# Optimization experiments

Hardware: AMD Instinct MI355X
Metric: run time of the kernel (lower is better)

The kernel has to match this reference:

```python
import jax, jax.numpy as jnp
import numpy as np

B, H, S, D = 2, 16, 2048, 64
DILATION_RATE = 2

def dilated_global_mask(seq_len: int, dilation_rate: int) -> jnp.ndarray:
    # mask[i, j] = 1 if |i - j| % dilation_rate == 0 else 0  -> [S, S] float32
    i = jnp.arange(seq_len)[:, None]
    j = jnp.arange(seq_len)[None, :]
    return ((jnp.abs(i - j) % dilation_rate) == 0).astype(jnp.float32)

def setup_inputs() -> dict:
    key = jax.random.key(0)
    kq, kk, kv = jax.random.split(key, 3)
    queries = jax.random.normal(kq, (B, H, S, D), dtype=jnp.float32)
    keys = jax.random.normal(kk, (B, H, S, D), dtype=jnp.float32)
    values = jax.random.normal(kv, (B, H, S, D), dtype=jnp.float32)
    return {"queries": queries, "keys": keys, "values": values}

def reference(queries, keys, values):
    depth = queries.shape[-1]
    # scores: [B, H, S, S]
    scores = jnp.einsum("bhqd,bhkd->bhqk", queries, keys)
    scores = scores / jnp.sqrt(jnp.asarray(depth, dtype=jnp.float32))
    gmask = dilated_global_mask(keys.shape[-2], DILATION_RATE)  # [S, S]
    # NOTE: multiplicative masking (masked scores become 0, not -inf), as in source
    masked_scores = scores * gmask
    attention_probs = jax.nn.softmax(masked_scores, axis=-1)
    # dropout is identity at inference (training=None)
    out = jnp.einsum("bhqk,bhkd->bhqd", attention_probs, values)
    return out
```

## Files before the change

### kernel.cpp

```cpp
#include <hip/hip_runtime.h>
#include <hip/hip_bf16.h>


#define B_   2
#define H_   16
#define S_   2048
#define D_   64
#define SP_  1024
#define BQ   128
#define BK   64
#define NKT  (SP_ / BK)
#define NW   4

#define QSCALE 0.180336884f

#if __has_builtin(__builtin_amdgcn_exp2f)
#define EXP2(x) __builtin_amdgcn_exp2f(x)
#else
#define EXP2(x) exp2f(x)
#endif

typedef __bf16 bf16x8 __attribute__((ext_vector_type(8)));
typedef __bf16 bf16x4 __attribute__((ext_vector_type(4)));
typedef float  f32x4  __attribute__((ext_vector_type(4)));
typedef short  s16x4  __attribute__((ext_vector_type(4)));

static __device__ __forceinline__ f32x4 mfma16(bf16x4 a, bf16x4 b, f32x4 c) {
    return __builtin_amdgcn_mfma_f32_16x16x16bf16_1k(
        __builtin_bit_cast(s16x4, a), __builtin_bit_cast(s16x4, b), c, 0, 0, 0);
}

#define KSW(r, c8) ((((c8) ^ ((r) & 7)) << 3))

__global__ __launch_bounds__(256, 2) void attn_kernel(const float* __restrict__ Q,
                                                      const float* __restrict__ K,
                                                      const float* __restrict__ V,
                                                      float* __restrict__ out) {
    const int bh  = blockIdx.x;
    const int par = blockIdx.y;
    const int qt  = blockIdx.z;
    const int tid  = threadIdx.x;
    const int lane = tid & 63;
    const int wave = tid >> 6;
    const int l15  = lane & 15;
    const int quad = lane >> 4;

    __shared__ __align__(16) char arena[33792];
    __bf16 (*kbuf)[BK][64] = (__bf16 (*)[BK][64])arena;
    __bf16 (*vbuf)[D_][64] = (__bf16 (*)[D_][64])(arena + 16384);
    float  (*vred)[64]     = (float  (*)[64])(arena + 32768);

    const size_t base = (size_t)bh * S_ * D_;
    const float* Qb = Q + base;
    const float* Kb = K + base;
    const float* Vb = V + base;
    const int vofs = (par == 0) ? D_ : -D_;

    bf16x8 qf[2][2];
    #pragma unroll
    for (int qt2 = 0; qt2 < 2; ++qt2) {
        const int qrow = qt * BQ + wave * 32 + qt2 * 16 + l15;
        const float* qsrc = Qb + (size_t)(par + 2 * qrow) * D_ + quad * 8;
        #pragma unroll
        for (int ks = 0; ks < 2; ++ks) {
            const float4 a = *(const float4*)(qsrc + ks * 32);
            const float4 b = *(const float4*)(qsrc + ks * 32 + 4);
            bf16x8 w;
            w[0] = (__bf16)(a.x * QSCALE); w[1] = (__bf16)(a.y * QSCALE);
            w[2] = (__bf16)(a.z * QSCALE); w[3] = (__bf16)(a.w * QSCALE);
            w[4] = (__bf16)(b.x * QSCALE); w[5] = (__bf16)(b.y * QSCALE);
            w[6] = (__bf16)(b.z * QSCALE); w[7] = (__bf16)(b.w * QSCALE);
            qf[qt2][ks] = w;
        }
    }

    const int kr0 = tid >> 3;
    const int kc8 = tid & 7;

    float4 pka[2], pkb[2];
    float  pv[16], pvo[16];

    auto issue_loads = [&](int kt) {
        #pragma unroll
        for (int i = 0; i < 2; ++i) {
            const int r = i * 32 + kr0;
            const float* ksrc = Kb + (size_t)(par + 2 * (kt * BK + r)) * D_ + kc8 * 8;
            pka[i] = *(const float4*)ksrc;
            pkb[i] = *(const float4*)(ksrc + 4);
        }
        #pragma unroll
        for (int i = 0; i < 2; ++i) {
            const int c = wave + 4 * i;
            const float* vsrc = Vb + (size_t)(par + 2 * (kt * BK + c * 8)) * D_ + lane;
            #pragma unroll
            for (int j = 0; j < 8; ++j) {
                pv [i * 8 + j] = vsrc[(size_t)(2 * j) * D_];
                pvo[i * 8 + j] = vsrc[(size_t)(2 * j) * D_ + vofs];
            }
        }
    };

    float vo = 0.f;
    auto stage = [&](int buf) {
        #pragma unroll
        for (int i = 0; i < 2; ++i) {
            const int r = i * 32 + kr0;
            bf16x8 w;
            w[0] = (__bf16)pka[i].x; w[1] = (__bf16)pka[i].y;
            w[2] = (__bf16)pka[i].z; w[3] = (__bf16)pka[i].w;
            w[4] = (__bf16)pkb[i].x; w[5] = (__bf16)pkb[i].y;
            w[6] = (__bf16)pkb[i].z; w[7] = (__bf16)pkb[i].w;
            *(bf16x8*)&kbuf[buf][r][KSW(r, kc8)] = w;
        }
        #pragma unroll
        for (int i = 0; i < 2; ++i) {
            const int c = wave + 4 * i;
            bf16x8 w;
            #pragma unroll
            for (int j = 0; j < 8; ++j) w[j] = (__bf16)pv[i * 8 + j];
            *(bf16x8*)&vbuf[buf][lane][KSW(lane, c)] = w;
            vo += ((pvo[i*8+0] + pvo[i*8+1]) + (pvo[i*8+2] + pvo[i*8+3]))
                + ((pvo[i*8+4] + pvo[i*8+5]) + (pvo[i*8+6] + pvo[i*8+7]));
        }
    };

    issue_loads(0);
    stage(0);
    __syncthreads();

    f32x4 acc[2][4];
    #pragma unroll
    for (int q2 = 0; q2 < 2; ++q2)
        #pragma unroll
        for (int dt = 0; dt < 4; ++dt) acc[q2][dt] = (f32x4){0.f, 0.f, 0.f, 0.f};
    float l_acc[2] = {0.f, 0.f};

    for (int kt = 0; kt < NKT; ++kt) {
        const int cur = kt & 1;
        const bool pf = (kt + 1 < NKT);

        if (pf) issue_loads(kt + 1);

        const __bf16 (*kb)[64] = kbuf[cur];
        const __bf16 (*vb)[64] = vbuf[cur];

        bf16x8 ka[2][4];
        #pragma unroll
        for (int ks = 0; ks < 2; ++ks)
            #pragma unroll
            for (int kt4 = 0; kt4 < 4; ++kt4) {
                const int R = kt4 * 16 + l15;
                ka[ks][kt4] = *(const bf16x8*)&kb[R][KSW(R, ks * 4 + quad)];
            }
        bf16x4 va[4][4];
        #pragma unroll
        for (int dt = 0; dt < 4; ++dt) {
            const int R = dt * 16 + l15;
            const int ro = R & 7;
            #pragma unroll
            for (int kt4 = 0; kt4 < 4; ++kt4) {
                const int ch = (kt4 * 2 + (quad >> 1)) ^ ro;
                va[kt4][dt] = *(const bf16x4*)&vb[R][ch * 8 + (quad & 1) * 4];
            }
        }

        #pragma unroll
        for (int qt2 = 0; qt2 < 2; ++qt2) {
            f32x4 st[4];
            #pragma unroll
            for (int kt4 = 0; kt4 < 4; ++kt4) st[kt4] = (f32x4){0.f, 0.f, 0.f, 0.f};
            #pragma unroll
            for (int ks = 0; ks < 2; ++ks)
                #pragma unroll
                for (int kt4 = 0; kt4 < 4; ++kt4)
                    st[kt4] = __builtin_amdgcn_mfma_f32_16x16x32_bf16(
                        ka[ks][kt4], qf[qt2][ks], st[kt4], 0, 0, 0);
            #pragma unroll
            for (int kt4 = 0; kt4 < 4; ++kt4) {
                const float p0 = EXP2(st[kt4][0]);
                const float p1 = EXP2(st[kt4][1]);
                const float p2 = EXP2(st[kt4][2]);
                const float p3 = EXP2(st[kt4][3]);
                l_acc[qt2] += (p0 + p1) + (p2 + p3);
                bf16x4 pb;
                pb[0] = (__bf16)p0; pb[1] = (__bf16)p1;
                pb[2] = (__bf16)p2; pb[3] = (__bf16)p3;
                #pragma unroll
                for (int dt = 0; dt < 4; ++dt)
                    acc[qt2][dt] = mfma16(va[kt4][dt], pb, acc[qt2][dt]);
            }
        }

        if (pf) stage(1 - cur);
        __syncthreads();
    }

    vred[wave][lane] = vo;
    __syncthreads();

    f32x4 vs4[4];
    #pragma unroll
    for (int dt = 0; dt < 4; ++dt) {
        f32x4 s = (f32x4){0.f, 0.f, 0.f, 0.f};
        #pragma unroll
        for (int w = 0; w < NW; ++w)
            s += *(const f32x4*)&vred[w][dt * 16 + quad * 4];
        vs4[dt] = s;
    }
    float rz[2];
    #pragma unroll
    for (int qt2 = 0; qt2 < 2; ++qt2) {
        float Z = l_acc[qt2];
        Z += __shfl_xor(Z, 16);
        Z += __shfl_xor(Z, 32);
        rz[qt2] = 1.0f / (Z + 1024.0f);
    }

    float* tw = (float*)arena + wave * (16 * 68);
    #pragma unroll
    for (int qt2 = 0; qt2 < 2; ++qt2) {
        #pragma unroll
        for (int dt = 0; dt < 4; ++dt) {
            const f32x4 o = (acc[qt2][dt] + vs4[dt]) * rz[qt2];
            *(f32x4*)&tw[l15 * 68 + dt * 16 + quad * 4] = o;
        }
        #pragma unroll
        for (int i = 0; i < 4; ++i) {
            const int q = i * 4 + quad;
            const f32x4 ov = *(const f32x4*)&tw[q * 68 + l15 * 4];
            const int qg = par + 2 * (qt * BQ + wave * 32 + qt2 * 16 + q);
            *(f32x4*)&out[base + (size_t)qg * D_ + l15 * 4] = ov;
        }
    }
}

extern "C" void kernel_launch(void* const* d_in, const int* in_sizes, int n_in,
                              void* d_out, int out_size, void* d_ws, size_t ws_size,
                              hipStream_t stream) {
    const float* Q = (const float*)d_in[0];
    const float* K = (const float*)d_in[1];
    const float* V = (const float*)d_in[2];
    float* out = (float*)d_out;
    attn_kernel<<<dim3(B_ * H_, 2, SP_ / BQ), dim3(256), 0, stream>>>(Q, K, V, out);
}
```

Measured before the change: 112.2 us.

## Use 8 waves per block with 16 query rows each instead of 4x32

```diff
diff --git a/kernel.cpp b/kernel.cpp
--- a/kernel.cpp
+++ b/kernel.cpp
@@ -10,7 +10,7 @@
 #define BQ   128
 #define BK   64
 #define NKT  (SP_ / BK)
-#define NW   4
+#define NW   8
 
 #define QSCALE 0.180336884f
 
@@ -32,7 +32,7 @@
 
 #define KSW(r, c8) ((((c8) ^ ((r) & 7)) << 3))
 
-__global__ __launch_bounds__(256, 2) void attn_kernel(const float* __restrict__ Q,
+__global__ __launch_bounds__(512, 4) void attn_kernel(const float* __restrict__ Q,
                                                       const float* __restrict__ K,
                                                       const float* __restrict__ V,
                                                       float* __restrict__ out) {
@@ -45,10 +45,10 @@
     const int l15  = lane & 15;
     const int quad = lane >> 4;
 
-    __shared__ __align__(16) char arena[33792];
+    __shared__ __align__(16) char arena[36864];
     __bf16 (*kbuf)[BK][64] = (__bf16 (*)[BK][64])arena;
     __bf16 (*vbuf)[D_][64] = (__bf16 (*)[D_][64])(arena + 16384);
-    float  (*vred)[64]     = (float  (*)[64])(arena + 32768);
+    float  (*vred)[64]     = (float  (*)[64])(arena + 34816);
 
     const size_t base = (size_t)bh * S_ * D_;
     const float* Qb = Q + base;
@@ -56,10 +56,9 @@
     const float* Vb = V + base;
     const int vofs = (par == 0) ? D_ : -D_;
 
-    bf16x8 qf[2][2];
-    #pragma unroll
-    for (int qt2 = 0; qt2 < 2; ++qt2) {
-        const int qrow = qt * BQ + wave * 32 + qt2 * 16 + l15;
+    bf16x8 qf[2];
+    {
+        const int qrow = qt * BQ + wave * 16 + l15;
         const float* qsrc = Qb + (size_t)(par + 2 * qrow) * D_ + quad * 8;
         #pragma unroll
         for (int ks = 0; ks < 2; ++ks) {
@@ -70,70 +69,52 @@
             w[2] = (__bf16)(a.z * QSCALE); w[3] = (__bf16)(a.w * QSCALE);
             w[4] = (__bf16)(b.x * QSCALE); w[5] = (__bf16)(b.y * QSCALE);
             w[6] = (__bf16)(b.z * QSCALE); w[7] = (__bf16)(b.w * QSCALE);
-            qf[qt2][ks] = w;
+            qf[ks] = w;
         }
     }
 
-    const int kr0 = tid >> 3;
+    const int kr  = tid >> 3;
     const int kc8 = tid & 7;
 
-    float4 pka[2], pkb[2];
-    float  pv[16], pvo[16];
+    float4 pka, pkb;
+    float  pv[8], pvo[8];
 
     auto issue_loads = [&](int kt) {
-        #pragma unroll
-        for (int i = 0; i < 2; ++i) {
-            const int r = i * 32 + kr0;
-            const float* ksrc = Kb + (size_t)(par + 2 * (kt * BK + r)) * D_ + kc8 * 8;
-            pka[i] = *(const float4*)ksrc;
-            pkb[i] = *(const float4*)(ksrc + 4);
-        }
-        #pragma unroll
-        for (int i = 0; i < 2; ++i) {
-            const int c = wave + 4 * i;
-            const float* vsrc = Vb + (size_t)(par + 2 * (kt * BK + c * 8)) * D_ + lane;
-            #pragma unroll
-            for (int j = 0; j < 8; ++j) {
-                pv [i * 8 + j] = vsrc[(size_t)(2 * j) * D_];
-                pvo[i * 8 + j] = vsrc[(size_t)(2 * j) * D_ + vofs];
-            }
+        const float* ksrc = Kb + (size_t)(par + 2 * (kt * BK + kr)) * D_ + kc8 * 8;
+        pka = *(const float4*)ksrc;
+        pkb = *(const float4*)(ksrc + 4);
+        const float* vsrc = Vb + (size_t)(par + 2 * (kt * BK + wave * 8)) * D_ + lane;
+        #pragma unroll
+        for (int j = 0; j < 8; ++j) {
+            pv [j] = vsrc[(size_t)(2 * j) * D_];
+            pvo[j] = vsrc[(size_t)(2 * j) * D_ + vofs];
         }
     };
 
     float vo = 0.f;
     auto stage = [&](int buf) {
-        #pragma unroll
-        for (int i = 0; i < 2; ++i) {
-            const int r = i * 32 + kr0;
-            bf16x8 w;
-            w[0] = (__bf16)pka[i].x; w[1] = (__bf16)pka[i].y;
-            w[2] = (__bf16)pka[i].z; w[3] = (__bf16)pka[i].w;
-            w[4] = (__bf16)pkb[i].x; w[5] = (__bf16)pkb[i].y;
-            w[6] = (__bf16)pkb[i].z; w[7] = (__bf16)pkb[i].w;
-            *(bf16x8*)&kbuf[buf][r][KSW(r, kc8)] = w;
-        }
-        #pragma unroll
-        for (int i = 0; i < 2; ++i) {
-            const int c = wave + 4 * i;
-            bf16x8 w;
-            #pragma unroll
-            for (int j = 0; j < 8; ++j) w[j] = (__bf16)pv[i * 8 + j];
-            *(bf16x8*)&vbuf[buf][lane][KSW(lane, c)] = w;
-            vo += ((pvo[i*8+0] + pvo[i*8+1]) + (pvo[i*8+2] + pvo[i*8+3]))
-                + ((pvo[i*8+4] + pvo[i*8+5]) + (pvo[i*8+6] + pvo[i*8+7]));
-        }
+        bf16x8 w;
+        w[0] = (__bf16)pka.x; w[1] = (__bf16)pka.y;
+        w[2] = (__bf16)pka.z; w[3] = (__bf16)pka.w;
+        w[4] = (__bf16)pkb.x; w[5] = (__bf16)pkb.y;
+        w[6] = (__bf16)pkb.z; w[7] = (__bf16)pkb.w;
+        *(bf16x8*)&kbuf[buf][kr][KSW(kr, kc8)] = w;
+        bf16x8 wv;
+        #pragma unroll
+        for (int j = 0; j < 8; ++j) wv[j] = (__bf16)pv[j];
+        *(bf16x8*)&vbuf[buf][lane][KSW(lane, wave)] = wv;
+        vo += ((pvo[0] + pvo[1]) + (pvo[2] + pvo[3]))
+            + ((pvo[4] + pvo[5]) + (pvo[6] + pvo[7]));
     };
 
     issue_loads(0);
     stage(0);
     __syncthreads();
 
-    f32x4 acc[2][4];
-    #pragma unroll
-    for (int q2 = 0; q2 < 2; ++q2)
-        #pragma unroll
-        for (int dt = 0; dt < 4; ++dt) acc[q2][dt] = (f32x4){0.f, 0.f, 0.f, 0.f};
-    float l_acc[2] = {0.f, 0.f};
+    f32x4 acc[4];
+    #pragma unroll
+    for (int dt = 0; dt < 4; ++dt) acc[dt] = (f32x4){0.f, 0.f, 0.f, 0.f};
+    float l_acc = 0.f;
 
     for (int kt = 0; kt < NKT; ++kt) {
         const int cur = kt & 1;
@@ -144,50 +125,34 @@
         const __bf16 (*kb)[64] = kbuf[cur];
         const __bf16 (*vb)[64] = vbuf[cur];
 
-        bf16x8 ka[2][4];
+        f32x4 st[4];
+        #pragma unroll
+        for (int kt4 = 0; kt4 < 4; ++kt4) st[kt4] = (f32x4){0.f, 0.f, 0.f, 0.f};
         #pragma unroll
         for (int ks = 0; ks < 2; ++ks)
             #pragma unroll
             for (int kt4 = 0; kt4 < 4; ++kt4) {
                 const int R = kt4 * 16 + l15;
-                ka[ks][kt4] = *(const bf16x8*)&kb[R][KSW(R, ks * 4 + quad)];
+                const bf16x8 a = *(const bf16x8*)&kb[R][KSW(R, ks * 4 + quad)];
+                st[kt4] = __builtin_amdgcn_mfma_f32_16x16x32_bf16(a, qf[ks], st[kt4], 0, 0, 0);
             }
-        bf16x4 va[4][4];
-        #pragma unroll
-        for (int dt = 0; dt < 4; ++dt) {
-            const int R = dt * 16 + l15;
-            const int ro = R & 7;
+
+        #pragma unroll
+        for (int kt4 = 0; kt4 < 4; ++kt4) {
+            const float p0 = EXP2(st[kt4][0]);
+            const float p1 = EXP2(st[kt4][1]);
+            const float p2 = EXP2(st[kt4][2]);
+            const float p3 = EXP2(st[kt4][3]);
+            l_acc += (p0 + p1) + (p2 + p3);
+            bf16x4 pb;
+            pb[0] = (__bf16)p0; pb[1] = (__bf16)p1;
+            pb[2] = (__bf16)p2; pb[3] = (__bf16)p3;
             #pragma unroll
-            for (int kt4 = 0; kt4 < 4; ++kt4) {
-                const int ch = (kt4 * 2 + (quad >> 1)) ^ ro;
-                va[kt4][dt] = *(const bf16x4*)&vb[R][ch * 8 + (quad & 1) * 4];
-            }
-        }
-
-        #pragma unroll
-        for (int qt2 = 0; qt2 < 2; ++qt2) {
-            f32x4 st[4];
-            #pragma unroll
-            for (int kt4 = 0; kt4 < 4; ++kt4) st[kt4] = (f32x4){0.f, 0.f, 0.f, 0.f};
-            #pragma unroll
-            for (int ks = 0; ks < 2; ++ks)
-                #pragma unroll
-                for (int kt4 = 0; kt4 < 4; ++kt4)
-                    st[kt4] = __builtin_amdgcn_mfma_f32_16x16x32_bf16(
-                        ka[ks][kt4], qf[qt2][ks], st[kt4], 0, 0, 0);
-            #pragma unroll
-            for (int kt4 = 0; kt4 < 4; ++kt4) {
-                const float p0 = EXP2(st[kt4][0]);
-                const float p1 = EXP2(st[kt4][1]);
-                const float p2 = EXP2(st[kt4][2]);
-                const float p3 = EXP2(st[kt4][3]);
-                l_acc[qt2] += (p0 + p1) + (p2 + p3);
-                bf16x4 pb;
-                pb[0] = (__bf16)p0; pb[1] = (__bf16)p1;
-                pb[2] = (__bf16)p2; pb[3] = (__bf16)p3;
-                #pragma unroll
-                for (int dt = 0; dt < 4; ++dt)
-                    acc[qt2][dt] = mfma16(va[kt4][dt], pb, acc[qt2][dt]);
+            for (int dt = 0; dt < 4; ++dt) {
+                const int R = dt * 16 + l15;
+                const int ch = (kt4 * 2 + (quad >> 1)) ^ (R & 7);
+                const bf16x4 va = *(const bf16x4*)&vb[R][ch * 8 + (quad & 1) * 4];
+                acc[dt] = mfma16(va, pb, acc[dt]);
             }
         }
 
@@ -207,30 +172,23 @@
             s += *(const f32x4*)&vred[w][dt * 16 + quad * 4];
         vs4[dt] = s;
     }
-    float rz[2];
-    #pragma unroll
-    for (int qt2 = 0; qt2 < 2; ++qt2) {
-        float Z = l_acc[qt2];
-        Z += __shfl_xor(Z, 16);
-        Z += __shfl_xor(Z, 32);
-        rz[qt2] = 1.0f / (Z + 1024.0f);
-    }
+    float Z = l_acc;
+    Z += __shfl_xor(Z, 16);
+    Z += __shfl_xor(Z, 32);
+    const float rz = 1.0f / (Z + 1024.0f);
 
     float* tw = (float*)arena + wave * (16 * 68);
     #pragma unroll
-    for (int qt2 = 0; qt2 < 2; ++qt2) {
-        #pragma unroll
-        for (int dt = 0; dt < 4; ++dt) {
-            const f32x4 o = (acc[qt2][dt] + vs4[dt]) * rz[qt2];
-            *(f32x4*)&tw[l15 * 68 + dt * 16 + quad * 4] = o;
-        }
-        #pragma unroll
-        for (int i = 0; i < 4; ++i) {
-            const int q = i * 4 + quad;
-            const f32x4 ov = *(const f32x4*)&tw[q * 68 + l15 * 4];
-            const int qg = par + 2 * (qt * BQ + wave * 32 + qt2 * 16 + q);
-            *(f32x4*)&out[base + (size_t)qg * D_ + l15 * 4] = ov;
-        }
+    for (int dt = 0; dt < 4; ++dt) {
+        const f32x4 o = (acc[dt] + vs4[dt]) * rz;
+        *(f32x4*)&tw[l15 * 68 + dt * 16 + quad * 4] = o;
+    }
+    #pragma unroll
+    for (int i = 0; i < 4; ++i) {
+        const int q = i * 4 + quad;
+        const f32x4 ov = *(const f32x4*)&tw[q * 68 + l15 * 4];
+        const int qg = par + 2 * (qt * BQ + wave * 16 + q);
+        *(f32x4*)&out[base + (size_t)qg * D_ + l15 * 4] = ov;
     }
 }
 
@@ -241,5 +199,5 @@
     const float* K = (const float*)d_in[1];
     const float* V = (const float*)d_in[2];
     float* out = (float*)d_out;
-    attn_kernel<<<dim3(B_ * H_, 2, SP_ / BQ), dim3(256), 0, stream>>>(Q, K, V, out);
+    attn_kernel<<<dim3(B_ * H_, 2, SP_ / BQ), dim3(512), 0, stream>>>(Q, K, V, out);
 }
```

Result: no change. 113.8 us (+1.4%).
